# Kernel optimization log

Hardware: AMD Instinct MI355X
Metric: run time of the kernel (lower is better)

## Reference

```python
import jax, jax.numpy as jnp
import numpy as np

HEAD_SIZE = 128

def setup_inputs() -> dict:
    key = jax.random.key(0)
    ks = jax.random.split(key, 4)
    B, T, C, H = 8, 2048, 1024, HEAD_SIZE
    x = jax.random.normal(ks[0], (B, T, C), dtype=jnp.float32)
    Wk = jax.random.normal(ks[1], (C, H), dtype=jnp.float32) * (C ** -0.5)
    Wq = jax.random.normal(ks[2], (C, H), dtype=jnp.float32) * (C ** -0.5)
    Wv = jax.random.normal(ks[3], (C, H), dtype=jnp.float32) * (C ** -0.5)
    return {"x": x, "Wk": Wk, "Wq": Wq, "Wv": Wv}

def reference(x, Wk, Wq, Wv):
    # x: [B,T,C]; projections to [B,T,H]
    k = jnp.einsum('btc,ch->bth', x, Wk)
    q = jnp.einsum('btc,ch->bth', x, Wq)
    v = jnp.einsum('btc,ch->bth', x, Wv)
    scale = HEAD_SIZE ** -0.5
    wei = jnp.einsum('bqh,bkh->bqk', q, k) * scale  # [B,T,T]
    T = x.shape[1]
    causal = jnp.tril(jnp.ones((T, T), dtype=bool))
    wei = jnp.where(causal, wei, -jnp.inf)
    wei = jax.nn.softmax(wei, axis=-1)
    # dropout p=0 (eval) -> identity
    out = jnp.einsum('bqk,bkh->bqh', wei, v)  # [B,T,H]
    return out
```

## Files before the change

kernel.cpp:

```cpp
#include <hip/hip_runtime.h>

#define B_DIM 8
#define T_DIM 2048
#define C_DIM 1024
#define H_DIM 128

typedef __attribute__((ext_vector_type(8))) short bf16x8;
typedef __attribute__((ext_vector_type(4))) float f32x4;

__device__ __forceinline__ short f2bf(float f) {
  union { float f; unsigned u; } v; v.f = f;
  unsigned u = v.u;
  unsigned r = (u + 0x7FFFu + ((u >> 16) & 1u)) >> 16;
  return (short)r;
}

__device__ __forceinline__ float rowmax16(float x) {
  union { float f; int i; } a, t;
  a.f = x;
  t.i = __builtin_amdgcn_update_dpp(a.i, a.i, 0x128, 0xf, 0xf, false);
  a.f = fmaxf(a.f, t.f);
  t.i = __builtin_amdgcn_update_dpp(a.i, a.i, 0x124, 0xf, 0xf, false);
  a.f = fmaxf(a.f, t.f);
  t.i = __builtin_amdgcn_update_dpp(a.i, a.i, 0x122, 0xf, 0xf, false);
  a.f = fmaxf(a.f, t.f);
  t.i = __builtin_amdgcn_update_dpp(a.i, a.i, 0x121, 0xf, 0xf, false);
  a.f = fmaxf(a.f, t.f);
  return a.f;
}
__device__ __forceinline__ float rowsum16(float x) {
  union { float f; int i; } a, t;
  a.f = x;
  t.i = __builtin_amdgcn_update_dpp(a.i, a.i, 0x128, 0xf, 0xf, false);
  a.f += t.f;
  t.i = __builtin_amdgcn_update_dpp(a.i, a.i, 0x124, 0xf, 0xf, false);
  a.f += t.f;
  t.i = __builtin_amdgcn_update_dpp(a.i, a.i, 0x122, 0xf, 0xf, false);
  a.f += t.f;
  t.i = __builtin_amdgcn_update_dpp(a.i, a.i, 0x121, 0xf, 0xf, false);
  a.f += t.f;
  return a.f;
}

#define NWE ((3 * C_DIM * H_DIM) / 8)

__global__ __launch_bounds__(256) void wprep_kernel(
    const float* __restrict__ Wk, const float* __restrict__ Wq,
    const float* __restrict__ Wv, short* __restrict__ Wtp) {
  int j = blockIdx.x * 256 + threadIdx.x;
  if (j >= NWE) return;
  int w = j >> 14;
  int r = j & 16383;
  int h = r >> 7;
  int c0 = (r & 127) * 8;
  const float* W = (w == 0) ? Wk : ((w == 1) ? Wq : Wv);
  __attribute__((aligned(16))) short t[8];
#pragma unroll
  for (int i = 0; i < 8; i++) t[i] = f2bf(W[(size_t)(c0 + i) * H_DIM + h]);
  int colg = w * 128 + h;
  int nt = colg >> 4, nn = colg & 15;
  int kc = c0 >> 5, quad = (c0 >> 3) & 3;
  *(int4*)(Wtp + ((size_t)(nt * 32 + kc) * 64 + quad * 16 + nn) * 8) =
      *(const int4*)t;
}

__global__ __launch_bounds__(512, 2) void projf_kernel(
    const float* __restrict__ x, const short* __restrict__ Wtp,
    short* __restrict__ Kp, short* __restrict__ Qb, short* __restrict__ Vp) {
  const int m0 = blockIdx.x * 32;
  __shared__ short As[2][32][72];
  const int tid  = threadIdx.x;
  const int lane = tid & 63;
  const int wv   = tid >> 6;
  const int n    = lane & 15;
  const int quad = lane >> 4;

  const int ar = tid >> 4, ac4 = (tid & 15) * 4;
  const float* xrow = x + (size_t)(m0 + ar) * C_DIM + ac4;
  const short* Bw = Wtp + (size_t)(wv * 3) * 32 * 512 + lane * 8;

  f32x4 acc[2][3];
#pragma unroll
  for (int i = 0; i < 2; i++)
#pragma unroll
    for (int j = 0; j < 3; j++) {
      f32x4 z = {0.f, 0.f, 0.f, 0.f};
      acc[i][j] = z;
    }

  float4 s0, s1;
  auto LOADA = [&](int it, float4& s) { s = *(const float4*)(xrow + it * 64); };
  auto STOREA = [&](int buf, const float4& s) {
    __attribute__((aligned(8))) short t4[4];
    t4[0] = f2bf(s.x); t4[1] = f2bf(s.y); t4[2] = f2bf(s.z); t4[3] = f2bf(s.w);
    *(int2*)&As[buf][ar][ac4] = *(const int2*)t4;
  };

  LOADA(0, s0);
  STOREA(0, s0);
  LOADA(1, s1);
  __syncthreads();

#pragma unroll 2
  for (int it = 0; it < 16; ++it) {
    bf16x8 bF[6], aF[4];
#pragma unroll
    for (int ntl = 0; ntl < 3; ntl++)
#pragma unroll
      for (int kk = 0; kk < 2; kk++)
        bF[ntl * 2 + kk] =
            *(const bf16x8*)(Bw + (size_t)(ntl * 32 + it * 2 + kk) * 512);
#pragma unroll
    for (int mt = 0; mt < 2; mt++)
#pragma unroll
      for (int kk = 0; kk < 2; kk++)
        aF[mt * 2 + kk] =
            *(const bf16x8*)&As[it & 1][mt * 16 + n][kk * 32 + quad * 8];
    __builtin_amdgcn_sched_barrier(0);
#pragma unroll
    for (int mt = 0; mt < 2; mt++)
#pragma unroll
      for (int ntl = 0; ntl < 3; ntl++)
#pragma unroll
        for (int kk = 0; kk < 2; kk++)
          acc[mt][ntl] = __builtin_amdgcn_mfma_f32_16x16x32_bf16(
              aF[mt * 2 + kk], bF[ntl * 2 + kk], acc[mt][ntl], 0, 0, 0);

    if (it < 15) {
      __syncthreads();
      if (((it + 1) & 1) == 0) STOREA(0, s0); else STOREA(1, s1);
      if (it + 2 < 16) {
        if (((it + 2) & 1) == 0) LOADA(it + 2, s0); else LOADA(it + 2, s1);
      }
      __syncthreads();
    }
  }

#pragma unroll
  for (int mt = 0; mt < 2; mt++) {
#pragma unroll
    for (int ntl = 0; ntl < 3; ntl++) {
#pragma unroll
      for (int i = 0; i < 4; i++) {
        int row = m0 + mt * 16 + quad * 4 + i;
        int col = wv * 48 + ntl * 16 + n;
        short v = f2bf(acc[mt][ntl][i]);
        int w = col >> 7;
        int c = col & 127;
        int bb = row >> 11;
        int t  = row & (T_DIM - 1);
        int tt = t >> 6;
        if (w == 0) {
          int rr = t & 63;
          int knt = rr >> 4, kn = rr & 15;
          int kc = c >> 5, kq = (c >> 3) & 3, kj = c & 7;
          Kp[(((size_t)(bb * 32 + tt) * 16 + knt * 4 + kc) * 512) +
             (kq * 16 + kn) * 8 + kj] = v;
        } else if (w == 1) {
          Qb[(size_t)row * H_DIM + c] = v;
        } else {
          int vkc = (t >> 5) & 1, vq = (t >> 3) & 3, vj = t & 7;
          int ht = c >> 4, vn = c & 15;
          Vp[(((size_t)(bb * 32 + tt) * 16 + ht * 2 + vkc) * 512) +
             (vq * 16 + vn) * 8 + vj] = v;
        }
      }
    }
  }
}

__global__ __launch_bounds__(256, 2) void attn_kernel(
    const short* __restrict__ Qb, const short* __restrict__ Kp,
    const short* __restrict__ Vp, float* __restrict__ out) {
  const int id = blockIdx.y * 128 + blockIdx.x;
  const int b  = id & 7;
  const int qt = 127 - (id >> 3);
  const int q0 = qt * 16;
  const int tid  = threadIdx.x;
  const int lane = tid & 63;
  const int g    = tid >> 6;
  const int n    = lane & 15;
  const int quad = lane >> 4;

  __shared__ short Ps[4][16][72];
  __shared__ float Om[16][128];
  __shared__ float Ml[16][2];

  const int ntiles = (qt >> 2) + 1;
  const float scale = 0.08838834764831845f;
  const int row0 = q0 + quad * 4;

  const short* Kbase = Kp + (size_t)b * 32 * 16 * 512;
  const short* Vbase = Vp + (size_t)b * 32 * 16 * 512;

  bf16x8 aQ[4];
  {
    const short* qrow = Qb + (size_t)(b * T_DIM + q0 + n) * H_DIM;
#pragma unroll
    for (int kc = 0; kc < 4; kc++)
      aQ[kc] = *(const bf16x8*)(qrow + kc * 32 + quad * 8);
  }

  f32x4 accO[8];
#pragma unroll
  for (int i = 0; i < 8; i++) {
    f32x4 z = {0.f, 0.f, 0.f, 0.f};
    accO[i] = z;
  }
  float mrow[4] = {-1e30f, -1e30f, -1e30f, -1e30f};
  float lrow[4] = {0.f, 0.f, 0.f, 0.f};

  for (int t = g; t < ntiles; t += 4) {
    const int j0 = t * 64;
    const short* Kt = Kbase + (size_t)t * 16 * 512 + lane * 8;
    const short* Vt = Vbase + (size_t)t * 16 * 512 + lane * 8;
    f32x4 accS[4];
#pragma unroll
    for (int nt = 0; nt < 4; nt++) {
      f32x4 z = {0.f, 0.f, 0.f, 0.f};
      accS[nt] = z;
    }
    bf16x8 fr[16];
#pragma unroll
    for (int nt = 0; nt < 4; nt++)
#pragma unroll
      for (int kc = 0; kc < 4; kc++)
        fr[nt * 4 + kc] = *(const bf16x8*)(Kt + (nt * 4 + kc) * 512);
    __builtin_amdgcn_sched_barrier(0);
#pragma unroll
    for (int nt = 0; nt < 4; nt++)
#pragma unroll
      for (int kc = 0; kc < 4; kc++)
        accS[nt] = __builtin_amdgcn_mfma_f32_16x16x32_bf16(
            aQ[kc], fr[nt * 4 + kc], accS[nt], 0, 0, 0);
    __builtin_amdgcn_sched_barrier(0);

    float mt4[4] = {-1e30f, -1e30f, -1e30f, -1e30f};
#pragma unroll
    for (int nt = 0; nt < 4; nt++) {
      int col = j0 + nt * 16 + n;
#pragma unroll
      for (int i = 0; i < 4; i++) {
        float s = accS[nt][i] * scale;
        s = (col > row0 + i) ? -1e30f : s;
        accS[nt][i] = s;
        mt4[i] = fmaxf(mt4[i], s);
      }
    }
#pragma unroll
    for (int i = 0; i < 4; i++) mt4[i] = rowmax16(mt4[i]);

    bf16x8 frv[8];
#pragma unroll
    for (int ht = 0; ht < 4; ht++)
#pragma unroll
      for (int kc = 0; kc < 2; kc++)
        frv[ht * 2 + kc] = *(const bf16x8*)(Vt + (ht * 2 + kc) * 512);
    __builtin_amdgcn_sched_barrier(0);

    float alpha[4], rsum[4];
#pragma unroll
    for (int i = 0; i < 4; i++) {
      float mnew = fmaxf(mrow[i], mt4[i]);
      alpha[i] = __expf(mrow[i] - mnew);
      mrow[i] = mnew;
      rsum[i] = 0.f;
    }
#pragma unroll
    for (int nt = 0; nt < 4; nt++)
#pragma unroll
      for (int i = 0; i < 4; i++) {
        float p = __expf(accS[nt][i] - mrow[i]);
        rsum[i] += p;
        Ps[g][quad * 4 + i][nt * 16 + n] = f2bf(p);
      }
#pragma unroll
    for (int i = 0; i < 4; i++) {
      rsum[i] = rowsum16(rsum[i]);
      lrow[i] = lrow[i] * alpha[i] + rsum[i];
    }
#pragma unroll
    for (int ht = 0; ht < 8; ht++)
#pragma unroll
      for (int i = 0; i < 4; i++)
        accO[ht][i] *= alpha[i];

    asm volatile("s_waitcnt lgkmcnt(0)" ::: "memory");
    __builtin_amdgcn_sched_barrier(0);

    bf16x8 aP[2];
#pragma unroll
    for (int kc = 0; kc < 2; kc++)
      aP[kc] = *(const bf16x8*)&Ps[g][n][kc * 32 + quad * 8];

#pragma unroll
    for (int ht = 0; ht < 4; ht++)
#pragma unroll
      for (int kc = 0; kc < 2; kc++)
        accO[ht] = __builtin_amdgcn_mfma_f32_16x16x32_bf16(
            aP[kc], frv[ht * 2 + kc], accO[ht], 0, 0, 0);
    __builtin_amdgcn_sched_barrier(0);
#pragma unroll
    for (int ht = 0; ht < 4; ht++)
#pragma unroll
      for (int kc = 0; kc < 2; kc++)
        frv[ht * 2 + kc] = *(const bf16x8*)(Vt + ((ht + 4) * 2 + kc) * 512);
    __builtin_amdgcn_sched_barrier(0);
#pragma unroll
    for (int ht = 0; ht < 4; ht++)
#pragma unroll
      for (int kc = 0; kc < 2; kc++)
        accO[ht + 4] = __builtin_amdgcn_mfma_f32_16x16x32_bf16(
            aP[kc], frv[ht * 2 + kc], accO[ht + 4], 0, 0, 0);
  }

  __syncthreads();
  if (g == 0) {
#pragma unroll
    for (int i = 0; i < 4; i++) {
      int r = quad * 4 + i;
#pragma unroll
      for (int ht = 0; ht < 8; ht++)
        Om[r][ht * 16 + n] = accO[ht][i];
      if (n == 0) { Ml[r][0] = mrow[i]; Ml[r][1] = lrow[i]; }
    }
  }
#pragma unroll
  for (int gg = 1; gg < 4; gg++) {
    __syncthreads();
    if (g == gg) {
#pragma unroll
      for (int i = 0; i < 4; i++) {
        int r = quad * 4 + i;
        float m1 = Ml[r][0], l1 = Ml[r][1];
        float mnew = fmaxf(mrow[i], m1);
        float a0 = __expf(mrow[i] - mnew);
        float a1 = __expf(m1 - mnew);
        float lnew = lrow[i] * a0 + l1 * a1;
        if (gg < 3) {
          if (n == 0) { Ml[r][0] = mnew; Ml[r][1] = lnew; }
#pragma unroll
          for (int ht = 0; ht < 8; ht++)
            Om[r][ht * 16 + n] = accO[ht][i] * a0 + Om[r][ht * 16 + n] * a1;
        } else {
          float linv = 1.0f / lnew;
          size_t base = (size_t)(b * T_DIM + q0 + r) * H_DIM;
#pragma unroll
          for (int ht = 0; ht < 8; ht++)
            out[base + ht * 16 + n] =
                (accO[ht][i] * a0 + Om[r][ht * 16 + n] * a1) * linv;
        }
      }
    }
  }
}

extern "C" void kernel_launch(void* const* d_in, const int* in_sizes, int n_in,
                              void* d_out, int out_size, void* d_ws, size_t ws_size,
                              hipStream_t stream) {
  (void)in_sizes; (void)n_in; (void)out_size; (void)ws_size;
  const float* x  = (const float*)d_in[0];
  const float* Wk = (const float*)d_in[1];
  const float* Wq = (const float*)d_in[2];
  const float* Wv = (const float*)d_in[3];
  float* out = (float*)d_out;

  char* ws = (char*)d_ws;
  short* Wtp = (short*)ws;
  short* Kp = (short*)(ws + 786432);
  short* Qb = (short*)(ws + 786432 + 4194304);
  short* Vp = (short*)(ws + 786432 + 8388608);

  wprep_kernel<<<dim3(192), dim3(256), 0, stream>>>(Wk, Wq, Wv, Wtp);
  projf_kernel<<<dim3(512), dim3(512), 0, stream>>>(x, Wtp, Kp, Qb, Vp);
  attn_kernel<<<dim3(128, 8), dim3(256), 0, stream>>>(Qb, Kp, Vp, out);
}
```

Baseline: 151.1 us.

## Stage full x tile in LDS once and drop per-iteration barriers in projection

The projection kernel now loads the whole 32x1024 fp32 slice of x into shared memory as bf16 up front, using wide 8-element loads. It then runs the 16 K-iterations with no barriers or double-buffer handoffs. This removes two __syncthreads per iteration and the serialized per-step global loads. The cost is about 66 KB of LDS per block, which may reduce occupancy below the declared 2 blocks/CU, and all global latency is exposed before any MFMA starts.

```diff
diff --git a/kernel.cpp b/kernel.cpp
--- a/kernel.cpp
+++ b/kernel.cpp
@@ -68,15 +68,35 @@
     const float* __restrict__ x, const short* __restrict__ Wtp,
     short* __restrict__ Kp, short* __restrict__ Qb, short* __restrict__ Vp) {
   const int m0 = blockIdx.x * 32;
-  __shared__ short As[2][32][72];
+  __shared__ short As[32][1056];
   const int tid  = threadIdx.x;
   const int lane = tid & 63;
   const int wv   = tid >> 6;
   const int n    = lane & 15;
   const int quad = lane >> 4;
 
-  const int ar = tid >> 4, ac4 = (tid & 15) * 4;
-  const float* xrow = x + (size_t)(m0 + ar) * C_DIM + ac4;
+  {
+    float4 xs[16];
+#pragma unroll
+    for (int k = 0; k < 8; k++) {
+      int c = tid + k * 512;
+      const float* src = x + (size_t)(m0 + (c >> 7)) * C_DIM + (c & 127) * 8;
+      xs[k * 2]     = *(const float4*)src;
+      xs[k * 2 + 1] = *(const float4*)(src + 4);
+    }
+#pragma unroll
+    for (int k = 0; k < 8; k++) {
+      int c = tid + k * 512;
+      __attribute__((aligned(16))) short t8[8];
+      t8[0] = f2bf(xs[k * 2].x);     t8[1] = f2bf(xs[k * 2].y);
+      t8[2] = f2bf(xs[k * 2].z);     t8[3] = f2bf(xs[k * 2].w);
+      t8[4] = f2bf(xs[k * 2 + 1].x); t8[5] = f2bf(xs[k * 2 + 1].y);
+      t8[6] = f2bf(xs[k * 2 + 1].z); t8[7] = f2bf(xs[k * 2 + 1].w);
+      *(int4*)&As[c >> 7][(c & 127) * 8] = *(const int4*)t8;
+    }
+  }
+  __syncthreads();
+
   const short* Bw = Wtp + (size_t)(wv * 3) * 32 * 512 + lane * 8;
 
   f32x4 acc[2][3];
@@ -88,20 +108,7 @@
       acc[i][j] = z;
     }
 
-  float4 s0, s1;
-  auto LOADA = [&](int it, float4& s) { s = *(const float4*)(xrow + it * 64); };
-  auto STOREA = [&](int buf, const float4& s) {
-    __attribute__((aligned(8))) short t4[4];
-    t4[0] = f2bf(s.x); t4[1] = f2bf(s.y); t4[2] = f2bf(s.z); t4[3] = f2bf(s.w);
-    *(int2*)&As[buf][ar][ac4] = *(const int2*)t4;
-  };
-
-  LOADA(0, s0);
-  STOREA(0, s0);
-  LOADA(1, s1);
-  __syncthreads();
-
-#pragma unroll 2
+#pragma unroll 4
   for (int it = 0; it < 16; ++it) {
     bf16x8 bF[6], aF[4];
 #pragma unroll
@@ -115,8 +122,7 @@
 #pragma unroll
       for (int kk = 0; kk < 2; kk++)
         aF[mt * 2 + kk] =
-            *(const bf16x8*)&As[it & 1][mt * 16 + n][kk * 32 + quad * 8];
-    __builtin_amdgcn_sched_barrier(0);
+            *(const bf16x8*)&As[mt * 16 + n][it * 64 + kk * 32 + quad * 8];
 #pragma unroll
     for (int mt = 0; mt < 2; mt++)
 #pragma unroll
@@ -125,15 +131,6 @@
         for (int kk = 0; kk < 2; kk++)
           acc[mt][ntl] = __builtin_amdgcn_mfma_f32_16x16x32_bf16(
               aF[mt * 2 + kk], bF[ntl * 2 + kk], acc[mt][ntl], 0, 0, 0);
-
-    if (it < 15) {
-      __syncthreads();
-      if (((it + 1) & 1) == 0) STOREA(0, s0); else STOREA(1, s1);
-      if (it + 2 < 16) {
-        if (((it + 2) & 1) == 0) LOADA(it + 2, s0); else LOADA(it + 2, s1);
-      }
-      __syncthreads();
-    }
   }
 
 #pragma unroll
```

New measurement: 144.8 us. -4.2%, faster.
